# Optimization experiments

Measured on AMD Instinct MI355X. Metric: run time of the kernel, lower is better.

## Reference

```python
import jax, jax.numpy as jnp
import numpy as np

# HGT meta: 2 node types (A=0, B=1), 3 relations (src_type, dst_type)
L, T, R = 3, 2, 3
H, D = 1, 64            # PyG HGTConv default heads=1, head_dim = hidden/heads
F = H * D               # hidden_channels = input feature dim = 64
NA = NB = 131072
E = 1_000_000
REL = [(0, 1), (1, 0), (0, 0)]


def setup_inputs() -> dict:
    key = jax.random.key(0)
    ks = jax.random.split(key, 16)
    sc = 1.0 / np.sqrt(F)
    inp = {}
    inp["xA"] = jax.random.normal(ks[0], (NA, F), jnp.float32)
    inp["xB"] = jax.random.normal(ks[1], (NB, F), jnp.float32)
    # K/Q/V projections per (layer, node_type)
    inp["Wk"] = jax.random.normal(ks[2], (L, T, F, F), jnp.float32) * sc
    inp["bk"] = jnp.zeros((L, T, F), jnp.float32)
    inp["Wq"] = jax.random.normal(ks[3], (L, T, F, F), jnp.float32) * sc
    inp["bq"] = jnp.zeros((L, T, F), jnp.float32)
    inp["Wv"] = jax.random.normal(ks[4], (L, T, F, F), jnp.float32) * sc
    inp["bv"] = jnp.zeros((L, T, F), jnp.float32)
    # per (layer, relation, head) attention / message matrices and priority
    inp["a_rel"] = jax.random.normal(ks[5], (L, R, H, D, D), jnp.float32) * sc
    inp["m_rel"] = jax.random.normal(ks[6], (L, R, H, D, D), jnp.float32) * sc
    inp["p_rel"] = jnp.ones((L, R, H), jnp.float32)
    # output projection + skip gate per (layer, node_type)
    inp["Wa"] = jax.random.normal(ks[7], (L, T, F, F), jnp.float32) * sc
    inp["ba"] = jnp.zeros((L, T, F), jnp.float32)
    inp["skip"] = jnp.ones((L, T), jnp.float32)
    # final readout Linear(hidden, 1)
    inp["lin_w"] = jax.random.normal(ks[8], (F, 1), jnp.float32) * sc
    inp["lin_b"] = jnp.zeros((1,), jnp.float32)
    # edge indices: ei[0]=src, ei[1]=dst (NA == NB so one range works)
    inp["ei1"] = jax.random.randint(ks[9], (2, E), 0, NA, jnp.int32)   # A -> B
    inp["ei2"] = jax.random.randint(ks[10], (2, E), 0, NA, jnp.int32)  # B -> A
    inp["ei3"] = jax.random.randint(ks[11], (2, E), 0, NA, jnp.int32)  # A -> A
    return inp


def _hgt_layer(xs, eis, Wk, bk, Wq, bq, Wv, bv, a_rel, m_rel, p_rel, Wa, ba, skip):
    # per-type K/Q/V projections, reshaped to [N, H, D]
    k = [(xs[t] @ Wk[t] + bk[t]).reshape(-1, H, D) for t in range(T)]
    q = [(xs[t] @ Wq[t] + bq[t]).reshape(-1, H, D) for t in range(T)]
    v = [(xs[t] @ Wv[t] + bv[t]).reshape(-1, H, D) for t in range(T)]
    agg = [jnp.zeros((xs[t].shape[0], H, D), xs[t].dtype) for t in range(T)]
    inv_sqrt_d = jnp.asarray(1.0 / np.sqrt(D), xs[0].dtype)
    for r, (s, d) in enumerate(REL):
        src, dst = eis[r][0], eis[r][1]
        n_d = xs[d].shape[0]
        # relation-specific transforms on source nodes, then edge gather
        k_r = jnp.einsum('nhd,hde->nhe', k[s], a_rel[r])
        v_r = jnp.einsum('nhd,hde->nhe', v[s], m_rel[r])
        # attention score per edge per head: (q_dst . k_src) * p_rel / sqrt(D)
        score = jnp.einsum('ehd,ehd->eh', q[d][dst], k_r[src]) * p_rel[r] * inv_sqrt_d
        # segment softmax over incoming edges of each dst node (per edge type)
        mx = jax.ops.segment_max(score, dst, num_segments=n_d)
        ex = jnp.exp(score - mx[dst])
        den = jax.ops.segment_sum(ex, dst, num_segments=n_d)
        alpha = ex / den[dst]                      # [E, H]
        msg = alpha[:, :, None] * v_r[src]         # [E, H, D]
        agg[d] = agg[d] + jax.ops.segment_sum(msg, dst, num_segments=n_d)
    outs = []
    for t in range(T):
        o = jax.nn.gelu(agg[t].reshape(-1, F), approximate=False) @ Wa[t] + ba[t]
        a = jax.nn.sigmoid(skip[t])               # skip gate (out_dim == in_dim)
        outs.append(a * o + (1.0 - a) * xs[t])
    return outs


def reference(xA, xB, Wk, bk, Wq, bq, Wv, bv, a_rel, m_rel, p_rel, Wa, ba, skip,
              lin_w, lin_b, ei1, ei2, ei3):
    xs = [xA, xB]
    eis = [ei1, ei2, ei3]
    for l in range(L):
        xs = _hgt_layer(xs, eis, Wk[l], bk[l], Wq[l], bq[l], Wv[l], bv[l],
                        a_rel[l], m_rel[l], p_rel[l], Wa[l], ba[l], skip[l])
    x = jnp.concatenate(xs, axis=0)               # concat all node types
    pooled = jnp.sum(x, axis=0, keepdims=True)    # global_add_pool, batch=None
    return pooled @ lin_w + lin_b                 # Linear(hidden, 1) -> [1, 1]
```

## Files before the change

kernel.cpp:

```cpp
#include <hip/hip_runtime.h>
#include <cmath>

#define DEV __device__ __forceinline__

typedef __attribute__((ext_vector_type(8))) short short8v;
typedef __attribute__((ext_vector_type(4))) float f32x4;

DEV float atomicAddF(float* p, float v) {
    return unsafeAtomicAdd(p, v);
}

DEV float gelu_exact(float v) {
    return 0.5f * v * (1.f + erff(v * 0.70710678118654752f));
}

DEV unsigned short f32_to_bf16(float f) {
    union { float f; unsigned int u; } x; x.f = f;
    unsigned int r = x.u + 0x7fffu + ((x.u >> 16) & 1u);
    return (unsigned short)(r >> 16);
}

DEV unsigned int f4_to_fp8x4(float a, float b, float c, float d) {
    int r = __builtin_amdgcn_cvt_pk_fp8_f32(a, b, 0, false);
    r = __builtin_amdgcn_cvt_pk_fp8_f32(c, d, r, true);
    return (unsigned int)r;
}

DEV float4 fp8x4_to_f4(unsigned int w) {
    auto lo = __builtin_amdgcn_cvt_pk_f32_fp8(w, false);
    auto hi = __builtin_amdgcn_cvt_pk_f32_fp8(w, true);
    return make_float4(lo[0], lo[1], hi[0], hi[1]);
}

DEV short8v cvt8_bf16(float4 f0, float4 f1) {
    union { unsigned int u[4]; short8v s; } r;
    asm("v_cvt_pk_bf16_f32 %0, %1, %2" : "=v"(r.u[0]) : "v"(f0.x), "v"(f0.y));
    asm("v_cvt_pk_bf16_f32 %0, %1, %2" : "=v"(r.u[1]) : "v"(f0.z), "v"(f0.w));
    asm("v_cvt_pk_bf16_f32 %0, %1, %2" : "=v"(r.u[2]) : "v"(f1.x), "v"(f1.y));
    asm("v_cvt_pk_bf16_f32 %0, %1, %2" : "=v"(r.u[3]) : "v"(f1.z), "v"(f1.w));
    return r.s;
}


struct MatSetB {
    const unsigned short* Wt[3];
    const float* b[3];
    float*       y[3];
    int          mode[3];
    int          n;
};

#define BCAP2 6144
#define SB_TILE 4096
#define PSTR 129

__global__ __launch_bounds__(256) void combine_w_bf16(
    const float* __restrict__ Wk, const float* __restrict__ bk,
    const float* __restrict__ Wv, const float* __restrict__ bv,
    const float* __restrict__ a_rel, const float* __restrict__ m_rel,
    const float* __restrict__ p_rel, unsigned short* __restrict__ CWt,
    float* __restrict__ Cb)
{
    const int r = blockIdx.x, kv = blockIdx.y, l = blockIdx.z;
    const int srcT[3] = {0, 1, 0};
    const int s = srcT[r];
    const float* Wsrc = (kv == 0 ? Wk : Wv) + ((size_t)(l*2 + s)) * 4096;
    const float* bsrc = (kv == 0 ? bk : bv) + ((size_t)(l*2 + s)) * 64;
    const float* A    = (kv == 0 ? a_rel : m_rel) + ((size_t)(l*3 + r)) * 4096;
    const float scale = (kv == 0) ? p_rel[l*3 + r] * 0.125f : 1.f;

    __shared__ float Ws[4096];
    __shared__ float As[4096];
    const int tid = threadIdx.x;
    for (int k = tid; k < 4096; k += 256) { Ws[k] = Wsrc[k]; As[k] = A[k]; }
    __syncthreads();

    unsigned short* out = CWt + ((size_t)(l*6 + r*2 + kv)) * 4096;
    const int j = tid & 63;
    #pragma unroll
    for (int i = 0; i < 16; i++) {
        const int f = (tid >> 6) * 16 + i;
        float acc = 0.f;
        #pragma unroll
        for (int e = 0; e < 64; e++) acc = fmaf(Ws[f*64 + e], As[e*64 + j], acc);
        const int so = (l == 0) ? f : (4*(f & 15) + (f >> 4));
        out[j*64 + so] = f32_to_bf16(acc * scale);
    }
    if (tid < 64) {
        float acc = 0.f;
        for (int e = 0; e < 64; e++) acc = fmaf(bsrc[e], As[e*64 + tid], acc);
        Cb[(size_t)(l*6 + r*2 + kv) * 64 + tid] = acc * scale;
    }
}

__global__ __launch_bounds__(256) void prep_wt(
    const float* __restrict__ Wq, const float* __restrict__ Wa,
    unsigned short* __restrict__ Wqt, unsigned short* __restrict__ Wat)
{
    const int bid = blockIdx.x;
    const float* src; unsigned short* dst; int useSigma;
    if (bid < 6) { src = Wq + (size_t)bid * 4096; dst = Wqt + (size_t)bid * 4096;
                   useSigma = (bid >= 2); }
    else         { src = Wa + (size_t)(bid - 6) * 4096; dst = Wat + (size_t)(bid - 6) * 4096;
                   useSigma = 1; }
    for (int idx = threadIdx.x; idx < 4096; idx += 256) {
        const int c = idx >> 6, s = idx & 63;
        const int k = useSigma ? (16*(s & 3) + (s >> 2)) : s;
        dst[c*64 + s] = f32_to_bf16(src[k*64 + c]);
    }
}

DEV void proj128_body(const float* __restrict__ x, const MatSetB& ms, int bid, int tid)
{
    const int wv  = tid >> 6;
    const int ln  = tid & 63;
    const int j   = ln & 15;
    const int g   = ln >> 4;
    const long long rowb = (long long)bid * 128 + wv * 32;

    short8v A[2][2];
    #pragma unroll
    for (int rg = 0; rg < 2; rg++) {
        const float* xp = x + (rowb + rg*16 + j) * 64 + g*8;
        #pragma unroll
        for (int ks = 0; ks < 2; ks++) {
            const float4 f0 = *(const float4*)(xp + ks*32);
            const float4 f1 = *(const float4*)(xp + ks*32 + 4);
            A[rg][ks] = cvt8_bf16(f0, f1);
        }
    }

    unsigned int kst[2][4];
    for (int m = 0; m < ms.n; m++) {
        short8v B[4][2];
        #pragma unroll
        for (int ct = 0; ct < 4; ct++) {
            const unsigned short* wp = ms.Wt[m] + (ct*16 + j) * 64 + g*8;
            B[ct][0] = *(const short8v*)(wp);
            B[ct][1] = *(const short8v*)(wp + 32);
        }
        f32x4 acc[2][4];
        #pragma unroll
        for (int ct = 0; ct < 4; ct++) {
            const float bm = ms.b[m][ct*16 + j];
            f32x4 bi = {bm, bm, bm, bm};
            acc[0][ct] = bi; acc[1][ct] = bi;
        }
        #pragma unroll
        for (int rg = 0; rg < 2; rg++)
            #pragma unroll
            for (int ct = 0; ct < 4; ct++) {
                acc[rg][ct] = __builtin_amdgcn_mfma_f32_16x16x32_bf16(
                    A[rg][0], B[ct][0], acc[rg][ct], 0, 0, 0);
                acc[rg][ct] = __builtin_amdgcn_mfma_f32_16x16x32_bf16(
                    A[rg][1], B[ct][1], acc[rg][ct], 0, 0, 0);
            }
        const int mode = ms.mode[m];
        if (mode == 0) {
            float* yb = ms.y[m];
            #pragma unroll
            for (int rg = 0; rg < 2; rg++)
                #pragma unroll
                for (int i = 0; i < 4; i++) {
                    const long long node = rowb + rg*16 + g*4 + i;
                    *(float4*)(yb + node*64 + j*4) = make_float4(
                        acc[rg][0][i], acc[rg][1][i], acc[rg][2][i], acc[rg][3][i]);
                }
        } else if (mode == 1) {
            #pragma unroll
            for (int rg = 0; rg < 2; rg++)
                #pragma unroll
                for (int i = 0; i < 4; i++)
                    kst[rg][i] = f4_to_fp8x4(
                        acc[rg][0][i], acc[rg][1][i], acc[rg][2][i], acc[rg][3][i]);
        } else {
            unsigned char* yb = (unsigned char*)ms.y[m];
            #pragma unroll
            for (int rg = 0; rg < 2; rg++)
                #pragma unroll
                for (int i = 0; i < 4; i++) {
                    const long long node = rowb + rg*16 + g*4 + i;
                    uint2 s;
                    s.x = kst[rg][i];
                    s.y = f4_to_fp8x4(
                        acc[rg][0][i], acc[rg][1][i], acc[rg][2][i], acc[rg][3][i]);
                    *(uint2*)(yb + node*128 + j*8) = s;
                }
        }
    }
}

__global__ __launch_bounds__(256) void proj_triple(
    const float* __restrict__ x1, MatSetB ms1, int g1,
    const float* __restrict__ x2, MatSetB ms2, int g2,
    const float* __restrict__ x3, MatSetB ms3)
{
    const int tid = threadIdx.x;
    int idx = blockIdx.x;
    if (idx < g1) { proj128_body(x1, ms1, idx, tid); return; }
    idx -= g1;
    if (idx < g2) { proj128_body(x2, ms2, idx, tid); return; }
    proj128_body(x3, ms3, idx - g2, tid);
}

__global__ __launch_bounds__(256) void scatter_bucket(
    const int* __restrict__ ei, int E, int nbuck,
    int* __restrict__ bcur, int2* __restrict__ pairbuf)
{
    __shared__ int  hist[256];
    __shared__ int  lbase[256];
    __shared__ int  gbase[256];
    __shared__ int  lcur[256];
    __shared__ int  scanbuf[256];
    __shared__ int2 stage[SB_TILE];
    const int tid = threadIdx.x;
    const int tile0 = blockIdx.x * SB_TILE;

    int2 my[16]; int mb[16];
    #pragma unroll
    for (int i = 0; i < 16; i++) {
        const int e = tile0 + tid + i*256;
        if (e < E) { my[i].x = ei[e]; my[i].y = ei[E + e]; mb[i] = my[i].y >> 9; }
        else mb[i] = -1;
    }
    hist[tid] = 0;
    __syncthreads();
    #pragma unroll
    for (int i = 0; i < 16; i++) if (mb[i] >= 0) atomicAdd(&hist[mb[i]], 1);
    __syncthreads();
    const int c = hist[tid];
    scanbuf[tid] = c;
    __syncthreads();
    for (int off = 1; off < 256; off <<= 1) {
        int add = (tid >= off) ? scanbuf[tid - off] : 0;
        __syncthreads();
        scanbuf[tid] += add;
        __syncthreads();
    }
    lbase[tid] = scanbuf[tid] - c;
    lcur[tid]  = scanbuf[tid] - c;
    if (c > 0 && tid < nbuck) gbase[tid] = atomicAdd(bcur + tid * 16, c);
    __syncthreads();
    #pragma unroll
    for (int i = 0; i < 16; i++) {
        if (mb[i] >= 0) {
            const int p = atomicAdd(&lcur[mb[i]], 1);
            stage[p] = my[i];
        }
    }
    __syncthreads();
    if (c > 0 && tid < nbuck) {
        const int gb = gbase[tid];
        const int lb = lbase[tid];
        int2* dstp = pairbuf + (size_t)tid * BCAP2;
        for (int jj = 0; jj < c; jj++) {
            const int gp = gb + jj;
            if (gp < BCAP2) dstp[gp] = stage[lb + jj];
        }
    }
}

__global__ __launch_bounds__(256) void bucket_csr(
    const int2* __restrict__ pairbuf, const int* __restrict__ bcur,
    int* __restrict__ row_ptr, int* __restrict__ row_end,
    int* __restrict__ col, int n)
{
    const int b   = blockIdx.x;
    const int tid = threadIdx.x;
    __shared__ int lcnt[512];
    __shared__ int lcur[512];
    __shared__ int scanbuf[256];
    int cnt = bcur[b * 16];
    if (cnt > BCAP2) cnt = BCAP2;
    lcnt[tid] = 0; lcnt[tid + 256] = 0;
    __syncthreads();
    const int2* src = pairbuf + (size_t)b * BCAP2;
    for (int i = tid; i < cnt; i += 256)
        atomicAdd(&lcnt[src[i].y & 511], 1);
    __syncthreads();
    const int c0 = lcnt[2*tid], c1 = lcnt[2*tid + 1];
    const int s = c0 + c1;
    scanbuf[tid] = s;
    __syncthreads();
    for (int off = 1; off < 256; off <<= 1) {
        int add = (tid >= off) ? scanbuf[tid - off] : 0;
        __syncthreads();
        scanbuf[tid] += add;
        __syncthreads();
    }
    const int excl = scanbuf[tid] - s;
    const int base = b * BCAP2;
    const int d0 = (b << 9) + 2*tid;
    if (d0 < n)     { row_ptr[d0]   = base + excl;      row_end[d0]   = base + excl + c0; }
    if (d0 + 1 < n) { row_ptr[d0+1] = base + excl + c0; row_end[d0+1] = base + excl + c0 + c1; }
    lcur[2*tid] = excl; lcur[2*tid + 1] = excl + c0;
    __syncthreads();
    for (int i = tid; i < cnt; i += 256) {
        const int2 p = src[i];
        const int pos = atomicAdd(&lcur[p.y & 511], 1);
        col[base + pos] = p.x;
    }
}

#define PROC_EDGE(KVR)                                                                 \
    {                                                                                  \
        const float4 ka_ = fp8x4_to_f4(KVR.x);                                         \
        const float4 kb2_ = fp8x4_to_f4(KVR.z);                                        \
        float sc_ = q0.x*ka_.x + q0.y*ka_.y + q0.z*ka_.z + q0.w*ka_.w                  \
                  + q1.x*kb2_.x + q1.y*kb2_.y + q1.z*kb2_.z + q1.w*kb2_.w;             \
        sc_ += __shfl_xor(sc_, 1); sc_ += __shfl_xor(sc_, 2); sc_ += __shfl_xor(sc_, 4);\
        const float p_ = __expf(sc_);                                                  \
        const float4 va_ = fp8x4_to_f4(KVR.y);                                         \
        const float4 vb_ = fp8x4_to_f4(KVR.w);                                         \
        ssum_ += p_;                                                                   \
        acc0_.x = fmaf(p_, va_.x, acc0_.x); acc0_.y = fmaf(p_, va_.y, acc0_.y);        \
        acc0_.z = fmaf(p_, va_.z, acc0_.z); acc0_.w = fmaf(p_, va_.w, acc0_.w);        \
        acc1_.x = fmaf(p_, vb_.x, acc1_.x); acc1_.y = fmaf(p_, vb_.y, acc1_.y);        \
        acc1_.z = fmaf(p_, vb_.z, acc1_.z); acc1_.w = fmaf(p_, vb_.w, acc1_.w);        \
    }

#define AGG_BODY(RP, RE, COL, KV, O0, O1)                                              \
    {                                                                                  \
        float4 acc0_ = {0.f,0.f,0.f,0.f}, acc1_ = {0.f,0.f,0.f,0.f};                   \
        float ssum_ = 0.f;                                                             \
        const int ss0_ = (RP)[dst], ss1_ = (RE)[dst];                                  \
        const unsigned char* kb_ = (KV) + sub*16;                                      \
        int e_ = ss0_;                                                                 \
        uint4 qq0_ = {0,0,0,0}, qq1_ = {0,0,0,0}, qq2_ = {0,0,0,0}, qq3_ = {0,0,0,0};  \
        if (e_ < ss1_)     qq0_ = *(const uint4*)(kb_ + (size_t)(COL)[e_] * 128);      \
        if (e_ + 1 < ss1_) qq1_ = *(const uint4*)(kb_ + (size_t)(COL)[e_+1] * 128);    \
        if (e_ + 2 < ss1_) qq2_ = *(const uint4*)(kb_ + (size_t)(COL)[e_+2] * 128);    \
        if (e_ + 3 < ss1_) qq3_ = *(const uint4*)(kb_ + (size_t)(COL)[e_+3] * 128);    \
        for (; e_ + 4 < ss1_; e_ += 2) {                                               \
            const int nn0_ = (COL)[e_+4];                                              \
            const int nn1_ = (e_ + 5 < ss1_) ? (COL)[e_+5] : nn0_;                     \
            const uint4 tt0_ = *(const uint4*)(kb_ + (size_t)nn0_ * 128);              \
            const uint4 tt1_ = *(const uint4*)(kb_ + (size_t)nn1_ * 128);              \
            PROC_EDGE(qq0_)                                                            \
            PROC_EDGE(qq1_)                                                            \
            qq0_ = qq2_; qq1_ = qq3_; qq2_ = tt0_; qq3_ = tt1_;                        \
        }                                                                              \
        if (e_ < ss1_)     PROC_EDGE(qq0_)                                             \
        if (e_ + 1 < ss1_) PROC_EDGE(qq1_)                                             \
        if (e_ + 2 < ss1_) PROC_EDGE(qq2_)                                             \
        if (e_ + 3 < ss1_) PROC_EDGE(qq3_)                                             \
        const float inv_ = (ssum_ > 0.f) ? 1.f / ssum_ : 0.f;                          \
        O0.x = fmaf(acc0_.x, inv_, O0.x); O0.y = fmaf(acc0_.y, inv_, O0.y);            \
        O0.z = fmaf(acc0_.z, inv_, O0.z); O0.w = fmaf(acc0_.w, inv_, O0.w);            \
        O1.x = fmaf(acc1_.x, inv_, O1.x); O1.y = fmaf(acc1_.y, inv_, O1.y);            \
        O1.z = fmaf(acc1_.z, inv_, O1.z); O1.w = fmaf(acc1_.w, inv_, O1.w);            \
    }

DEV void agg_block(
    const int* __restrict__ rp1, const int* __restrict__ re1, const int* __restrict__ c1,
    const int* __restrict__ rp2, const int* __restrict__ re2, const int* __restrict__ c2,
    const float* __restrict__ q,
    const unsigned char* __restrict__ kva, const unsigned char* __restrict__ kvb,
    float* __restrict__ xio, const unsigned short* __restrict__ Wat,
    const float* __restrict__ ba, const float* __restrict__ skipw,
    int xstd, int dual, int dopool, float* __restrict__ vec,
    int bid, int tid, float* lds, float* lds_pool)
{
    const long long rowb = (long long)bid * 128;
    if (tid < 64) lds_pool[tid] = 0.f;

    {
        const int sub = tid & 7;
        const int dl  = tid >> 3;
        const int dst = (int)rowb + dl;
        const float4* qp = (const float4*)(q + (size_t)dst * 64);
        const float4 q0 = qp[sub*2], q1 = qp[sub*2 + 1];
        float4 o0 = {0.f,0.f,0.f,0.f}, o1 = {0.f,0.f,0.f,0.f};
        AGG_BODY(rp1, re1, c1, kva, o0, o1)
        if (dual) {
            AGG_BODY(rp2, re2, c2, kvb, o0, o1)
        }
        float* lp = lds + (size_t)(8*sub) * PSTR + dl;
        lp[0*PSTR] = gelu_exact(o0.x); lp[1*PSTR] = gelu_exact(o0.y);
        lp[2*PSTR] = gelu_exact(o0.z); lp[3*PSTR] = gelu_exact(o0.w);
        lp[4*PSTR] = gelu_exact(o1.x); lp[5*PSTR] = gelu_exact(o1.y);
        lp[6*PSTR] = gelu_exact(o1.z); lp[7*PSTR] = gelu_exact(o1.w);
    }
    __syncthreads();

    if (tid < 512) {
        const int wv = tid >> 6;
        const int ln = tid & 63;
        const int j  = ln & 15;
        const int g  = ln >> 4;
        const int r  = wv*16 + j;

        short8v A[2];
        #pragma unroll
        for (int ks = 0; ks < 2; ks++) {
            const int pb = g*8 + ks*32;
            const float4 f0 = make_float4(lds[(pb+0)*PSTR + r], lds[(pb+1)*PSTR + r],
                                          lds[(pb+2)*PSTR + r], lds[(pb+3)*PSTR + r]);
            const float4 f1 = make_float4(lds[(pb+4)*PSTR + r], lds[(pb+5)*PSTR + r],
                                          lds[(pb+6)*PSTR + r], lds[(pb+7)*PSTR + r]);
            A[ks] = cvt8_bf16(f0, f1);
        }

        f32x4 acc[4];
        #pragma unroll
        for (int ct = 0; ct < 4; ct++) {
            const float bm = ba[ct*16 + j];
            acc[ct] = (f32x4){bm, bm, bm, bm};
        }
        #pragma unroll
        for (int ct = 0; ct < 4; ct++) {
            const unsigned short* wp = Wat + (ct*16 + j) * 64 + g*8;
            const short8v B0 = *(const short8v*)(wp);
            const short8v B1 = *(const short8v*)(wp + 32);
            acc[ct] = __builtin_amdgcn_mfma_f32_16x16x32_bf16(A[0], B0, acc[ct], 0, 0, 0);
            acc[ct] = __builtin_amdgcn_mfma_f32_16x16x32_bf16(A[1], B1, acc[ct], 0, 0, 0);
        }

        const float gate = 1.f / (1.f + __expf(-skipw[0]));
        const float og   = 1.f - gate;
        float4 pacc = {0.f,0.f,0.f,0.f};
        #pragma unroll
        for (int i = 0; i < 4; i++) {
            const long long node = rowb + wv*16 + g*4 + i;
            float* xp = xio + node*64;
            float4 o;
            if (xstd) {
                o.x = gate*acc[0][i] + og*xp[j];
                o.y = gate*acc[1][i] + og*xp[16 + j];
                o.z = gate*acc[2][i] + og*xp[32 + j];
                o.w = gate*acc[3][i] + og*xp[48 + j];
            } else {
                const float4 xo = *(const float4*)(xp + 4*j);
                o = make_float4(gate*acc[0][i] + og*xo.x,
                                gate*acc[1][i] + og*xo.y,
                                gate*acc[2][i] + og*xo.z,
                                gate*acc[3][i] + og*xo.w);
            }
            if (!dopool) {
                *(float4*)(xp + 4*j) = o;
            } else {
                pacc.x += o.x; pacc.y += o.y; pacc.z += o.z; pacc.w += o.w;
            }
        }
        if (dopool) {
            atomicAdd(&lds_pool[4*j + 0], pacc.x);
            atomicAdd(&lds_pool[4*j + 1], pacc.y);
            atomicAdd(&lds_pool[4*j + 2], pacc.z);
            atomicAdd(&lds_pool[4*j + 3], pacc.w);
        }
    }
    __syncthreads();
    if (dopool && tid < 64) atomicAddF(vec + tid, lds_pool[tid]);
}

__global__ __launch_bounds__(1024, 8) void agg_all(
    const int* __restrict__ rp0, const int* __restrict__ re0, const int* __restrict__ c0,
    const float* __restrict__ qB, const unsigned char* __restrict__ kv0,
    float* __restrict__ xB, const unsigned short* __restrict__ WatB,
    const float* __restrict__ baB, const float* __restrict__ skipB,
    const int* __restrict__ rp1, const int* __restrict__ re1, const int* __restrict__ c1,
    const int* __restrict__ rp2, const int* __restrict__ re2, const int* __restrict__ c2,
    const float* __restrict__ qA, const unsigned char* __restrict__ kv1,
    const unsigned char* __restrict__ kv2,
    float* __restrict__ xA, const unsigned short* __restrict__ WatA,
    const float* __restrict__ baA, const float* __restrict__ skipA,
    int xstd, int dopool, float* __restrict__ vec, int aggB, int aggA)
{
    __shared__ float lds[64 * PSTR];
    __shared__ float lds_pool[64];
    const int idx = blockIdx.x;
    const int tid = threadIdx.x;
    const int half = (aggA < aggB) ? aggA : aggB;
    int isDual, bid;
    if (idx < 2*half) { isDual = !(idx & 1); bid = idx >> 1; }
    else              { bid = idx - half;    isDual = (aggA > aggB); }
    if (isDual) {
        agg_block(rp1, re1, c1, rp2, re2, c2, qA, kv1, kv2, xA, WatA, baA, skipA,
                  xstd, 1, dopool, vec, bid, tid, lds, lds_pool);
    } else {
        agg_block(rp0, re0, c0, rp0, re0, c0, qB, kv0, kv0, xB, WatB, baB, skipB,
                  xstd, 0, dopool, vec, bid, tid, lds, lds_pool);
    }
}

__global__ void final_dot(const float* __restrict__ vec, const float* __restrict__ lw,
                          const float* __restrict__ lb, float* __restrict__ out)
{
    const int i = threadIdx.x;
    float v = vec[i] * lw[16*(i & 3) + (i >> 2)];
    #pragma unroll
    for (int m = 32; m >= 1; m >>= 1) v += __shfl_xor(v, m);
    if (i == 0) out[0] = v + lb[0];
}

extern "C" void kernel_launch(void* const* d_in, const int* in_sizes, int n_in,
                              void* d_out, int out_size, void* d_ws, size_t ws_size,
                              hipStream_t stream)
{
    float* xs[2] = {(float*)d_in[0], (float*)d_in[1]};
    const float* Wk    = (const float*)d_in[2];
    const float* bk    = (const float*)d_in[3];
    const float* Wq    = (const float*)d_in[4];
    const float* bq    = (const float*)d_in[5];
    const float* Wv    = (const float*)d_in[6];
    const float* bv    = (const float*)d_in[7];
    const float* a_rel = (const float*)d_in[8];
    const float* m_rel = (const float*)d_in[9];
    const float* p_rel = (const float*)d_in[10];
    const float* Wa    = (const float*)d_in[11];
    const float* ba    = (const float*)d_in[12];
    const float* skipw = (const float*)d_in[13];
    const float* lin_w = (const float*)d_in[14];
    const float* lin_b = (const float*)d_in[15];
    const int*   ei[3] = {(const int*)d_in[16], (const int*)d_in[17], (const int*)d_in[18]};

    const long long NA = in_sizes[0] / 64;
    const long long NB = in_sizes[1] / 64;
    const long long Ns[2] = {NA, NB};
    const long long Nmax = NA > NB ? NA : NB;
    int E[3];
    for (int r = 0; r < 3; r++) E[r] = in_sizes[16 + r] / 2;
    static const int dstN_is_B[3] = {1, 0, 0};
    const long long nbuckMax = (Nmax + 511) >> 9;

    float* w = (float*)d_ws;
    float* qB  = w; w += Nmax * 64;
    float* qA  = w; w += Nmax * 64;
    unsigned char* kv0 = (unsigned char*)w; w += Nmax * 32;
    unsigned char* kv1 = (unsigned char*)w; w += Nmax * 32;
    unsigned char* kv2 = (unsigned char*)w; w += Nmax * 32;
    unsigned short* CWt = (unsigned short*)w; w += 18 * 2048;
    unsigned short* Wqt = (unsigned short*)w; w += 6 * 2048;
    unsigned short* Wat = (unsigned short*)w; w += 6 * 2048;
    float* Cb    = w; w += 18 * 64;
    float* vec   = w; w += 64;
    int* iw = (int*)w;
    int* row_ptr[3]; int* row_end[3]; int* col[3];
    for (int r = 0; r < 3; r++) {
        row_ptr[r] = iw; iw += Nmax;
        row_end[r] = iw; iw += Nmax;
        col[r]     = iw; iw += nbuckMax * BCAP2;
    }
    int*  bcur    = iw; iw += nbuckMax * 16;
    int2* pairbuf = (int2*)iw;

    combine_w_bf16<<<dim3(3, 2, 3), 256, 0, stream>>>(Wk, bk, Wv, bv, a_rel, m_rel, p_rel, CWt, Cb);
    prep_wt<<<12, 256, 0, stream>>>(Wq, Wa, Wqt, Wat);
    hipMemsetAsync(vec, 0, 64 * sizeof(float), stream);

    for (int r = 0; r < 3; r++) {
        const int n = (int)Ns[dstN_is_B[r]];
        const int nbuck = (n + 511) >> 9;
        hipMemsetAsync(bcur, 0, (size_t)nbuck * 16 * sizeof(int), stream);
        scatter_bucket<<<(E[r] + SB_TILE - 1) / SB_TILE, 256, 0, stream>>>(
            ei[r], E[r], nbuck, bcur, pairbuf);
        bucket_csr<<<nbuck, 256, 0, stream>>>(pairbuf, bcur, row_ptr[r], row_end[r], col[r], n);
    }

    const int gA = (int)(NA >> 7), gB = (int)(NB >> 7);
    const int aggB = (int)(NB >> 7);
    const int aggA = (int)(NA >> 7);
    for (int l = 0; l < 3; l++) {
        const int xstd   = (l == 0) ? 1 : 0;
        const int dopool = (l == 2) ? 1 : 0;
        {
            MatSetB msB; msB.n = 3;
            msB.Wt[0] = Wqt + (size_t)(l*2 + 1) * 4096;  msB.b[0] = bq + (size_t)(l*2 + 1) * 64;
            msB.y[0] = qB;         msB.mode[0] = 0;
            msB.Wt[1] = CWt + (size_t)(l*6 + 2) * 4096;  msB.b[1] = Cb + (size_t)(l*6 + 2) * 64;
            msB.y[1] = nullptr;    msB.mode[1] = 1;
            msB.Wt[2] = CWt + (size_t)(l*6 + 3) * 4096;  msB.b[2] = Cb + (size_t)(l*6 + 3) * 64;
            msB.y[2] = (float*)kv1; msB.mode[2] = 2;
            MatSetB msA; msA.n = 2;
            msA.Wt[0] = CWt + (size_t)(l*6 + 0) * 4096;  msA.b[0] = Cb + (size_t)(l*6 + 0) * 64;
            msA.y[0] = nullptr;    msA.mode[0] = 1;
            msA.Wt[1] = CWt + (size_t)(l*6 + 1) * 4096;  msA.b[1] = Cb + (size_t)(l*6 + 1) * 64;
            msA.y[1] = (float*)kv0; msA.mode[1] = 2;
            msA.Wt[2] = msA.Wt[1]; msA.b[2] = msA.b[1]; msA.y[2] = msA.y[1]; msA.mode[2] = 2;
            MatSetB msA2; msA2.n = 3;
            msA2.Wt[0] = Wqt + (size_t)(l*2 + 0) * 4096;  msA2.b[0] = bq + (size_t)(l*2 + 0) * 64;
            msA2.y[0] = qA;         msA2.mode[0] = 0;
            msA2.Wt[1] = CWt + (size_t)(l*6 + 4) * 4096;  msA2.b[1] = Cb + (size_t)(l*6 + 4) * 64;
            msA2.y[1] = nullptr;    msA2.mode[1] = 1;
            msA2.Wt[2] = CWt + (size_t)(l*6 + 5) * 4096;  msA2.b[2] = Cb + (size_t)(l*6 + 5) * 64;
            msA2.y[2] = (float*)kv2; msA2.mode[2] = 2;
            proj_triple<<<gB + gA + gA, 256, 0, stream>>>(
                xs[1], msB, gB, xs[0], msA, gA, xs[0], msA2);
        }
        agg_all<<<aggB + aggA, 1024, 0, stream>>>(
            row_ptr[0], row_end[0], col[0], qB, kv0, xs[1],
            Wat + (size_t)(l*2 + 1) * 4096, ba + (size_t)(l*2 + 1) * 64, skipw + l*2 + 1,
            row_ptr[1], row_end[1], col[1],
            row_ptr[2], row_end[2], col[2],
            qA, kv1, kv2, xs[0],
            Wat + (size_t)(l*2 + 0) * 4096, ba + (size_t)(l*2 + 0) * 64, skipw + l*2 + 0,
            xstd, dopool, vec, aggB, aggA);
    }

    final_dot<<<1, 64, 0, stream>>>(vec, lin_w, lin_b, (float*)d_out);
}
```

Measured before the change: 816.1 us.

## Merge edge bucketing with layer-0 projection and batch CSR builds into single launches

The three relations' edge scatter passes now run in one launch together with the layer-0 K/Q/V projection blocks, and the three CSR builds run in one combined launch. Each relation gets its own bucket counter and pair buffer so they can proceed concurrently. This replaces several small serial launches and memsets with fewer, fuller grids, so the bucketing and projection work overlap. Bucket capacity is cut to 4608 to fit three pair buffers in the workspace, which raises the risk of silently dropping edges if a destination bucket overflows (mean is about 3900 per bucket).

```diff
diff --git a/kernel.cpp b/kernel.cpp
--- a/kernel.cpp
+++ b/kernel.cpp
@@ -50,7 +50,7 @@
     int          n;
 };
 
-#define BCAP2 6144
+#define BCAP2 4608
 #define SB_TILE 4096
 #define PSTR 129
 
@@ -203,9 +203,9 @@
     proj128_body(x3, ms3, idx - g2, tid);
 }
 
-__global__ __launch_bounds__(256) void scatter_bucket(
-    const int* __restrict__ ei, int E, int nbuck,
-    int* __restrict__ bcur, int2* __restrict__ pairbuf)
+struct ScatP { const int* ei; int E; int nbuck; int* bcur; int2* pb; int nblk; };
+
+DEV void scatter_body(const ScatP& sp, int bid, int tid)
 {
     __shared__ int  hist[256];
     __shared__ int  lbase[256];
@@ -213,8 +213,9 @@
     __shared__ int  lcur[256];
     __shared__ int  scanbuf[256];
     __shared__ int2 stage[SB_TILE];
-    const int tid = threadIdx.x;
-    const int tile0 = blockIdx.x * SB_TILE;
+    const int tile0 = bid * SB_TILE;
+    const int E = sp.E;
+    const int* ei = sp.ei;
 
     int2 my[16]; int mb[16];
     #pragma unroll
@@ -239,7 +240,7 @@
     }
     lbase[tid] = scanbuf[tid] - c;
     lcur[tid]  = scanbuf[tid] - c;
-    if (c > 0 && tid < nbuck) gbase[tid] = atomicAdd(bcur + tid * 16, c);
+    if (c > 0 && tid < sp.nbuck) gbase[tid] = atomicAdd(sp.bcur + tid * 16, c);
     __syncthreads();
     #pragma unroll
     for (int i = 0; i < 16; i++) {
@@ -249,10 +250,10 @@
         }
     }
     __syncthreads();
-    if (c > 0 && tid < nbuck) {
+    if (c > 0 && tid < sp.nbuck) {
         const int gb = gbase[tid];
         const int lb = lbase[tid];
-        int2* dstp = pairbuf + (size_t)tid * BCAP2;
+        int2* dstp = sp.pb + (size_t)tid * BCAP2;
         for (int jj = 0; jj < c; jj++) {
             const int gp = gb + jj;
             if (gp < BCAP2) dstp[gp] = stage[lb + jj];
@@ -260,21 +261,38 @@
     }
 }
 
-__global__ __launch_bounds__(256) void bucket_csr(
-    const int2* __restrict__ pairbuf, const int* __restrict__ bcur,
-    int* __restrict__ row_ptr, int* __restrict__ row_end,
-    int* __restrict__ col, int n)
-{
-    const int b   = blockIdx.x;
+__global__ __launch_bounds__(256) void proj_scatter(
+    ScatP s0, ScatP s1, ScatP s2,
+    const float* __restrict__ x1, MatSetB ms1, int g1,
+    const float* __restrict__ x2, MatSetB ms2, int g2,
+    const float* __restrict__ x3, MatSetB ms3)
+{
     const int tid = threadIdx.x;
+    int idx = blockIdx.x;
+    if (idx < s0.nblk) { scatter_body(s0, idx, tid); return; }
+    idx -= s0.nblk;
+    if (idx < s1.nblk) { scatter_body(s1, idx, tid); return; }
+    idx -= s1.nblk;
+    if (idx < s2.nblk) { scatter_body(s2, idx, tid); return; }
+    idx -= s2.nblk;
+    if (idx < g1) { proj128_body(x1, ms1, idx, tid); return; }
+    idx -= g1;
+    if (idx < g2) { proj128_body(x2, ms2, idx, tid); return; }
+    proj128_body(x3, ms3, idx - g2, tid);
+}
+
+struct CsrP { const int2* pb; const int* bcur; int* rp; int* re; int* col; int n; int nblk; };
+
+DEV void csr_body(const CsrP& cp, int b, int tid)
+{
     __shared__ int lcnt[512];
     __shared__ int lcur[512];
     __shared__ int scanbuf[256];
-    int cnt = bcur[b * 16];
+    int cnt = cp.bcur[b * 16];
     if (cnt > BCAP2) cnt = BCAP2;
     lcnt[tid] = 0; lcnt[tid + 256] = 0;
     __syncthreads();
-    const int2* src = pairbuf + (size_t)b * BCAP2;
+    const int2* src = cp.pb + (size_t)b * BCAP2;
     for (int i = tid; i < cnt; i += 256)
         atomicAdd(&lcnt[src[i].y & 511], 1);
     __syncthreads();
@@ -291,15 +309,25 @@
     const int excl = scanbuf[tid] - s;
     const int base = b * BCAP2;
     const int d0 = (b << 9) + 2*tid;
-    if (d0 < n)     { row_ptr[d0]   = base + excl;      row_end[d0]   = base + excl + c0; }
-    if (d0 + 1 < n) { row_ptr[d0+1] = base + excl + c0; row_end[d0+1] = base + excl + c0 + c1; }
+    if (d0 < cp.n)     { cp.rp[d0]   = base + excl;      cp.re[d0]   = base + excl + c0; }
+    if (d0 + 1 < cp.n) { cp.rp[d0+1] = base + excl + c0; cp.re[d0+1] = base + excl + c0 + c1; }
     lcur[2*tid] = excl; lcur[2*tid + 1] = excl + c0;
     __syncthreads();
     for (int i = tid; i < cnt; i += 256) {
         const int2 p = src[i];
         const int pos = atomicAdd(&lcur[p.y & 511], 1);
-        col[base + pos] = p.x;
-    }
+        cp.col[base + pos] = p.x;
+    }
+}
+
+__global__ __launch_bounds__(256) void csr_all(CsrP c0, CsrP c1, CsrP c2)
+{
+    const int tid = threadIdx.x;
+    int idx = blockIdx.x;
+    if (idx < c0.nblk) { csr_body(c0, idx, tid); return; }
+    idx -= c0.nblk;
+    if (idx < c1.nblk) { csr_body(c1, idx, tid); return; }
+    csr_body(c2, idx - c1.nblk, tid);
 }
 
 #define PROC_EDGE(KVR)                                                                 \
@@ -541,51 +569,74 @@
         row_end[r] = iw; iw += Nmax;
         col[r]     = iw; iw += nbuckMax * BCAP2;
     }
-    int*  bcur    = iw; iw += nbuckMax * 16;
-    int2* pairbuf = (int2*)iw;
+    int* bcur_all = iw; iw += 3 * nbuckMax * 16;
+    int2* pb_all  = (int2*)iw;
 
     combine_w_bf16<<<dim3(3, 2, 3), 256, 0, stream>>>(Wk, bk, Wv, bv, a_rel, m_rel, p_rel, CWt, Cb);
     prep_wt<<<12, 256, 0, stream>>>(Wq, Wa, Wqt, Wat);
     hipMemsetAsync(vec, 0, 64 * sizeof(float), stream);
-
-    for (int r = 0; r < 3; r++) {
-        const int n = (int)Ns[dstN_is_B[r]];
-        const int nbuck = (n + 511) >> 9;
-        hipMemsetAsync(bcur, 0, (size_t)nbuck * 16 * sizeof(int), stream);
-        scatter_bucket<<<(E[r] + SB_TILE - 1) / SB_TILE, 256, 0, stream>>>(
-            ei[r], E[r], nbuck, bcur, pairbuf);
-        bucket_csr<<<nbuck, 256, 0, stream>>>(pairbuf, bcur, row_ptr[r], row_end[r], col[r], n);
-    }
+    hipMemsetAsync(bcur_all, 0, (size_t)3 * nbuckMax * 16 * sizeof(int), stream);
 
     const int gA = (int)(NA >> 7), gB = (int)(NB >> 7);
     const int aggB = (int)(NB >> 7);
     const int aggA = (int)(NA >> 7);
+
+    MatSetB msB[3], msA[3], msA2[3];
+    for (int l = 0; l < 3; l++) {
+        msB[l].n = 3;
+        msB[l].Wt[0] = Wqt + (size_t)(l*2 + 1) * 4096;  msB[l].b[0] = bq + (size_t)(l*2 + 1) * 64;
+        msB[l].y[0] = qB;         msB[l].mode[0] = 0;
+        msB[l].Wt[1] = CWt + (size_t)(l*6 + 2) * 4096;  msB[l].b[1] = Cb + (size_t)(l*6 + 2) * 64;
+        msB[l].y[1] = nullptr;    msB[l].mode[1] = 1;
+        msB[l].Wt[2] = CWt + (size_t)(l*6 + 3) * 4096;  msB[l].b[2] = Cb + (size_t)(l*6 + 3) * 64;
+        msB[l].y[2] = (float*)kv1; msB[l].mode[2] = 2;
+        msA[l].n = 2;
+        msA[l].Wt[0] = CWt + (size_t)(l*6 + 0) * 4096;  msA[l].b[0] = Cb + (size_t)(l*6 + 0) * 64;
+        msA[l].y[0] = nullptr;    msA[l].mode[0] = 1;
+        msA[l].Wt[1] = CWt + (size_t)(l*6 + 1) * 4096;  msA[l].b[1] = Cb + (size_t)(l*6 + 1) * 64;
+        msA[l].y[1] = (float*)kv0; msA[l].mode[1] = 2;
+        msA[l].Wt[2] = msA[l].Wt[1]; msA[l].b[2] = msA[l].b[1];
+        msA[l].y[2] = msA[l].y[1];  msA[l].mode[2] = 2;
+        msA2[l].n = 3;
+        msA2[l].Wt[0] = Wqt + (size_t)(l*2 + 0) * 4096;  msA2[l].b[0] = bq + (size_t)(l*2 + 0) * 64;
+        msA2[l].y[0] = qA;         msA2[l].mode[0] = 0;
+        msA2[l].Wt[1] = CWt + (size_t)(l*6 + 4) * 4096;  msA2[l].b[1] = Cb + (size_t)(l*6 + 4) * 64;
+        msA2[l].y[1] = nullptr;    msA2[l].mode[1] = 1;
+        msA2[l].Wt[2] = CWt + (size_t)(l*6 + 5) * 4096;  msA2[l].b[2] = Cb + (size_t)(l*6 + 5) * 64;
+        msA2[l].y[2] = (float*)kv2; msA2[l].mode[2] = 2;
+    }
+
+    ScatP sp[3];
+    for (int r = 0; r < 3; r++) {
+        sp[r].ei    = ei[r];
+        sp[r].E     = E[r];
+        sp[r].nbuck = (int)((Ns[dstN_is_B[r]] + 511) >> 9);
+        sp[r].bcur  = bcur_all + (size_t)r * nbuckMax * 16;
+        sp[r].pb    = pb_all + (size_t)r * nbuckMax * BCAP2;
+        sp[r].nblk  = (E[r] + SB_TILE - 1) / SB_TILE;
+    }
+    proj_scatter<<<sp[0].nblk + sp[1].nblk + sp[2].nblk + gB + gA + gA, 256, 0, stream>>>(
+        sp[0], sp[1], sp[2],
+        xs[1], msB[0], gB, xs[0], msA[0], gA, xs[0], msA2[0]);
+
+    CsrP cp[3];
+    for (int r = 0; r < 3; r++) {
+        cp[r].pb   = sp[r].pb;
+        cp[r].bcur = sp[r].bcur;
+        cp[r].rp   = row_ptr[r];
+        cp[r].re   = row_end[r];
+        cp[r].col  = col[r];
+        cp[r].n    = (int)Ns[dstN_is_B[r]];
+        cp[r].nblk = sp[r].nbuck;
+    }
+    csr_all<<<cp[0].nblk + cp[1].nblk + cp[2].nblk, 256, 0, stream>>>(cp[0], cp[1], cp[2]);
+
     for (int l = 0; l < 3; l++) {
         const int xstd   = (l == 0) ? 1 : 0;
         const int dopool = (l == 2) ? 1 : 0;
-        {
-            MatSetB msB; msB.n = 3;
-            msB.Wt[0] = Wqt + (size_t)(l*2 + 1) * 4096;  msB.b[0] = bq + (size_t)(l*2 + 1) * 64;
-            msB.y[0] = qB;         msB.mode[0] = 0;
-            msB.Wt[1] = CWt + (size_t)(l*6 + 2) * 4096;  msB.b[1] = Cb + (size_t)(l*6 + 2) * 64;
-            msB.y[1] = nullptr;    msB.mode[1] = 1;
-            msB.Wt[2] = CWt + (size_t)(l*6 + 3) * 4096;  msB.b[2] = Cb + (size_t)(l*6 + 3) * 64;
-            msB.y[2] = (float*)kv1; msB.mode[2] = 2;
-            MatSetB msA; msA.n = 2;
-            msA.Wt[0] = CWt + (size_t)(l*6 + 0) * 4096;  msA.b[0] = Cb + (size_t)(l*6 + 0) * 64;
-            msA.y[0] = nullptr;    msA.mode[0] = 1;
-            msA.Wt[1] = CWt + (size_t)(l*6 + 1) * 4096;  msA.b[1] = Cb + (size_t)(l*6 + 1) * 64;
-            msA.y[1] = (float*)kv0; msA.mode[1] = 2;
-            msA.Wt[2] = msA.Wt[1]; msA.b[2] = msA.b[1]; msA.y[2] = msA.y[1]; msA.mode[2] = 2;
-            MatSetB msA2; msA2.n = 3;
-            msA2.Wt[0] = Wqt + (size_t)(l*2 + 0) * 4096;  msA2.b[0] = bq + (size_t)(l*2 + 0) * 64;
-            msA2.y[0] = qA;         msA2.mode[0] = 0;
-            msA2.Wt[1] = CWt + (size_t)(l*6 + 4) * 4096;  msA2.b[1] = Cb + (size_t)(l*6 + 4) * 64;
-            msA2.y[1] = nullptr;    msA2.mode[1] = 1;
-            msA2.Wt[2] = CWt + (size_t)(l*6 + 5) * 4096;  msA2.b[2] = Cb + (size_t)(l*6 + 5) * 64;
-            msA2.y[2] = (float*)kv2; msA2.mode[2] = 2;
+        if (l > 0) {
             proj_triple<<<gB + gA + gA, 256, 0, stream>>>(
-                xs[1], msB, gB, xs[0], msA, gA, xs[0], msA2);
+                xs[1], msB[l], gB, xs[0], msA[l], gA, xs[0], msA2[l]);
         }
         agg_all<<<aggB + aggA, 1024, 0, stream>>>(
             row_ptr[0], row_end[0], col[0], qB, kv0, xs[1],
```

After: 762.8 us. 1.07x faster.
